# Kernel optimization log

Measured on AMD Instinct MI355X. Metric: run time of the kernel, lower is better.

The kernel has to match this reference:

```python
import jax, jax.numpy as jnp
import numpy as np

TOP_K = 2
TEMP = 0.9
EPS = 1e-5
B, S, D, F, E = 2, 2048, 1024, 4096, 8


def setup_inputs() -> dict:
    key = jax.random.key(0)
    ks = jax.random.split(key, 4)
    scale_in = 1.0 / np.sqrt(D)
    scale_ff = 1.0 / np.sqrt(F)
    return {
        "x": jax.random.normal(ks[0], (B, S, D), jnp.float32),
        "gate_w": jax.random.normal(ks[1], (D, E), jnp.float32) * scale_in,
        "gate_b": jnp.zeros((E,), jnp.float32),
        "w1": jax.random.normal(ks[2], (E, D, F), jnp.float32) * scale_in,
        "b1": jnp.zeros((E, F), jnp.float32),
        "w2": jax.random.normal(ks[3], (E, F, D), jnp.float32) * scale_ff,
        "b2": jnp.zeros((E, D), jnp.float32),
        "ln_g": jnp.ones((D,), jnp.float32),
        "ln_b": jnp.zeros((D,), jnp.float32),
    }


def _moe_forward(x, gate_w, gate_b, w1, b1, w2, b2, ln_g, ln_b):
    # Gating: top-k masked softmax over experts
    logits = (x @ gate_w + gate_b) / TEMP                       # [B,S,E]
    topk_vals, topk_idx = jax.lax.top_k(logits, TOP_K)          # [B,S,K]
    keep = jax.nn.one_hot(topk_idx, E, dtype=jnp.bool_).any(-2)  # [B,S,E]
    masked = jnp.where(keep, logits, -jnp.inf)
    gate_probs = jax.nn.softmax(masked, axis=-1)                # [B,S,E]

    # Dense all-expert FFN (faithful to the naive original)
    h = jnp.einsum('bsd,edf->bsef', x, w1) + b1                 # [B,S,E,F]
    h = jax.nn.gelu(h, approximate=False)
    expert_out = jnp.einsum('bsef,efd->bsed', h, w2) + b2       # [B,S,E,D]

    out = jnp.einsum('bse,bsed->bsd', gate_probs, expert_out)   # combine

    # Post LayerNorm (dropout is identity in eval)
    mu = out.mean(-1, keepdims=True)
    var = out.var(-1, keepdims=True)
    out = (out - mu) / jnp.sqrt(var + EPS) * ln_g + ln_b
    return out


def reference(x, gate_w, gate_b, w1, b1, w2, b2, ln_g, ln_b):
    return _moe_forward(x, gate_w, gate_b, w1, b1, w2, b2, ln_g, ln_b)
```

## Files before the change

kernel.cpp:

```cpp
#include <hip/hip_runtime.h>
#include <stdint.h>
#include <stddef.h>

#define T_TOK 4096
#define DD    1024
#define FF    4096
#define EE    8
#define MAXROWS 9216
#define MAXTILES 72

typedef unsigned short u16;
typedef unsigned int   u32;
typedef short  sh8 __attribute__((ext_vector_type(8)));
typedef __bf16 bf8 __attribute__((ext_vector_type(8)));
typedef float  fl4 __attribute__((ext_vector_type(4)));

__device__ __forceinline__ u32 f2b_u(float f){
  u32 u = __float_as_uint(f);
  return (u + 0x7FFFu + ((u >> 16) & 1u)) >> 16;
}
__device__ __forceinline__ u16 f2b(float f){ return (u16)f2b_u(f); }
__device__ __forceinline__ u32 pack2(float a, float b){ return f2b_u(a) | (f2b_u(b) << 16); }

__device__ __forceinline__ void gl_lds16(const u16* g, u16* l){
  __builtin_amdgcn_global_load_lds(
      (const __attribute__((address_space(1))) u32*)(g),
      (__attribute__((address_space(3))) u32*)(l), 16, 0, 0);
}

__device__ __forceinline__ fl4 mfma16(sh8 a, sh8 b, fl4 c){
  return __builtin_amdgcn_mfma_f32_16x16x32_bf16(
      __builtin_bit_cast(bf8, a), __builtin_bit_cast(bf8, b), c, 0, 0, 0);
}

__device__ __forceinline__ float gelu_f(float x){
  float x2 = x * x;
  float t  = fmaf(0.07135481283f, x2, 1.5957691216f);
  float u  = x * t;
  float e  = __expf(-u);
  return x * __frcp_rn(1.0f + e);
}

__global__ __launch_bounds__(256) void k_cvt_x(const float* __restrict__ x,
                                               u16* __restrict__ xb){
  size_t i = ((size_t)blockIdx.x * 256 + threadIdx.x) * 8;
  float4 a = *(const float4*)(x + i);
  float4 b = *(const float4*)(x + i + 4);
  uint4 v;
  v.x = pack2(a.x, a.y); v.y = pack2(a.z, a.w);
  v.z = pack2(b.x, b.y); v.w = pack2(b.z, b.w);
  *(uint4*)(xb + i) = v;
}

__global__ __launch_bounds__(256) void k_gate(const float* __restrict__ x,
    const float* __restrict__ gw, const float* __restrict__ gb,
    int* __restrict__ tidx, float* __restrict__ tp, int* __restrict__ meta){
  int lane = threadIdx.x & 63;
  int t = blockIdx.x * 4 + (threadIdx.x >> 6);
  const float* xr = x + (size_t)t * DD;
  float a0=0,a1=0,a2=0,a3=0,a4=0,a5=0,a6=0,a7=0;
  #pragma unroll
  for (int i = 0; i < 16; i++){
    int d = i * 64 + lane;
    float xv = xr[d];
    const float4* g4 = (const float4*)(gw + (size_t)d * EE);
    float4 p = g4[0], q = g4[1];
    a0 += xv*p.x; a1 += xv*p.y; a2 += xv*p.z; a3 += xv*p.w;
    a4 += xv*q.x; a5 += xv*q.y; a6 += xv*q.z; a7 += xv*q.w;
  }
  #pragma unroll
  for (int off = 32; off > 0; off >>= 1){
    a0 += __shfl_xor(a0, off, 64); a1 += __shfl_xor(a1, off, 64);
    a2 += __shfl_xor(a2, off, 64); a3 += __shfl_xor(a3, off, 64);
    a4 += __shfl_xor(a4, off, 64); a5 += __shfl_xor(a5, off, 64);
    a6 += __shfl_xor(a6, off, 64); a7 += __shfl_xor(a7, off, 64);
  }
  if (lane == 0){
    float l[8] = {a0,a1,a2,a3,a4,a5,a6,a7};
    #pragma unroll
    for (int e = 0; e < 8; e++) l[e] = (l[e] + gb[e]) * (1.0f / 0.9f);
    int i1 = 0;
    #pragma unroll
    for (int e = 1; e < 8; e++) if (l[e] > l[i1]) i1 = e;
    int i2 = (i1 == 0) ? 1 : 0;
    #pragma unroll
    for (int e = 0; e < 8; e++) if (e != i1 && l[e] > l[i2]) i2 = e;
    float ex = expf(l[i2] - l[i1]);
    float inv = 1.0f / (1.0f + ex);
    tidx[2*t] = i1; tidx[2*t+1] = i2;
    tp[2*t] = inv;  tp[2*t+1] = ex * inv;
    atomicAdd(&meta[i1], 1);
    atomicAdd(&meta[i2], 1);
  }
}

__global__ __launch_bounds__(256) void k_fillscan(const int* __restrict__ tidx,
    const float* __restrict__ tp, int* __restrict__ meta,
    int* __restrict__ rowmap, float* __restrict__ rowp){
  __shared__ int sbase[EE];
  __shared__ int scur[EE];
  int tid = threadIdx.x;
  if (tid < EE) scur[tid] = 0;
  if (tid == 0){
    int rowbase = 0, total = 0;
    for (int e = 0; e < EE; e++){
      int c = meta[e];
      sbase[e] = rowbase;
      int nt = (c + 127) >> 7;
      for (int i = 0; i < nt; i++){
        meta[32 + total]  = e;
        meta[104 + total] = rowbase + i * 128;
        total++;
      }
      rowbase += nt << 7;
    }
    meta[24] = total;
  }
  __syncthreads();
  for (int t = tid; t < T_TOK; t += 256){
    #pragma unroll
    for (int k = 0; k < 2; k++){
      int e = tidx[2*t + k];
      int pos = atomicAdd(&scur[e], 1);
      int row = sbase[e] + pos;
      rowmap[row] = (t << 1) | k;
      rowp[row] = tp[2*t + k];
    }
  }
}

__global__ __launch_bounds__(256) void k_cvtw(const float* __restrict__ src,
    u16* __restrict__ dst, int R, int C){
  __shared__ float tile[64][65];
  int e = blockIdx.z;
  const float* se = src + (size_t)e * R * C;
  u16* de = dst + (size_t)e * R * C;
  int rblk = blockIdx.y * 64, cblk = blockIdx.x * 64;
  int tid = threadIdx.x;
  int lr = tid >> 4, lc = tid & 15;
  #pragma unroll
  for (int i = 0; i < 4; i++){
    int row = lr + i * 16;
    float4 v = *(const float4*)(se + (size_t)(rblk + row) * C + cblk + lc * 4);
    tile[row][lc*4+0] = v.x; tile[row][lc*4+1] = v.y;
    tile[row][lc*4+2] = v.z; tile[row][lc*4+3] = v.w;
  }
  __syncthreads();
  int c = tid >> 2, seg = tid & 3;
  u32 o[8];
  #pragma unroll
  for (int j = 0; j < 8; j++){
    float f0 = tile[seg*16 + 2*j    ][c];
    float f1 = tile[seg*16 + 2*j + 1][c];
    o[j] = pack2(f0, f1);
  }
  u16* dp = de + (size_t)(cblk + c) * R + rblk + seg * 16;
  *(uint4*)(dp)     = make_uint4(o[0], o[1], o[2], o[3]);
  *(uint4*)(dp + 8) = make_uint4(o[4], o[5], o[6], o[7]);
}

__global__ __launch_bounds__(256) void k_gemm_h(
    const u16* __restrict__ Xb, const u16* __restrict__ Wt,
    const float* __restrict__ b1, const int* __restrict__ meta,
    const int* __restrict__ rowmap, u16* __restrict__ H){
  __shared__ u16 As[128 * 64];
  __shared__ u16 Bs[128 * 64];
  int tx = blockIdx.x;
  if (tx >= meta[24]) return;
  int e = meta[32 + tx], row0 = meta[104 + tx];
  int n0 = blockIdx.y * 128;
  int tid = threadIdx.x;
  int rsub = tid >> 3;
  int sw_st = ((tid & 7) ^ (rsub & 7)) * 8;
  const u16* Be = Wt + ((size_t)e * FF + n0) * DD;
  const u16* gA[4];
  const u16* gB[4];
  #pragma unroll
  for (int j = 0; j < 4; j++){
    int row = j * 32 + rsub;
    int rm = rowmap[row0 + row];
    int tok = (rm < 0) ? 0 : (rm >> 1);
    gA[j] = Xb + (size_t)tok * DD + sw_st;
    gB[j] = Be + (size_t)row * DD + sw_st;
  }
  u16* lA = As + tid * 8;
  u16* lB = Bs + tid * 8;

  int lane = tid & 63, wv = tid >> 6;
  int wm = wv & 1, wn = wv >> 1;
  int lr = lane & 15, lq = lane >> 4;
  int sw0 = ((lq    ) ^ (lr & 7)) * 8;
  int sw1 = ((lq + 4) ^ (lr & 7)) * 8;
  const u16* pA = As + (wm * 64 + lr) * 64;
  const u16* pB = Bs + (wn * 64 + lr) * 64;

  fl4 acc[4][4];
  #pragma unroll
  for (int mi = 0; mi < 4; mi++)
    #pragma unroll
    for (int ni = 0; ni < 4; ni++) acc[mi][ni] = (fl4){0.f,0.f,0.f,0.f};

  for (int k0 = 0; k0 < DD; k0 += 64){
    #pragma unroll
    for (int j = 0; j < 4; j++){
      gl_lds16(gA[j] + k0, lA + j * 2048);
      gl_lds16(gB[j] + k0, lB + j * 2048);
    }
    __syncthreads();
    #pragma unroll
    for (int kk = 0; kk < 2; kk++){
      int sw = kk ? sw1 : sw0;
      sh8 a[4], b[4];
      #pragma unroll
      for (int mi = 0; mi < 4; mi++) a[mi] = *(const sh8*)(pA + mi * 1024 + sw);
      #pragma unroll
      for (int ni = 0; ni < 4; ni++) b[ni] = *(const sh8*)(pB + ni * 1024 + sw);
      #pragma unroll
      for (int mi = 0; mi < 4; mi++)
        #pragma unroll
        for (int ni = 0; ni < 4; ni++)
          acc[mi][ni] = mfma16(a[mi], b[ni], acc[mi][ni]);
    }
    __syncthreads();
  }

  const float* b1e = b1 + (size_t)e * FF;
  float bias[4];
  #pragma unroll
  for (int ni = 0; ni < 4; ni++) bias[ni] = b1e[n0 + wn*64 + ni*16 + lr];
  #pragma unroll
  for (int mi = 0; mi < 4; mi++){
    int grb = row0 + wm * 64 + mi * 16 + lq * 4;
    #pragma unroll
    for (int ni = 0; ni < 4; ni++){
      int gc = n0 + wn * 64 + ni * 16 + lr;
      #pragma unroll
      for (int r = 0; r < 4; r++){
        float v = acc[mi][ni][r] + bias[ni];
        H[(size_t)(grb + r) * FF + gc] = f2b(gelu_f(v));
      }
    }
  }
}

__global__ __launch_bounds__(256) void k_gemm_y(
    const u16* __restrict__ H, const u16* __restrict__ Wt,
    const float* __restrict__ b2, const int* __restrict__ meta,
    const int* __restrict__ rowmap, const float* __restrict__ rowp,
    float* __restrict__ slots){
  __shared__ u16 As[128 * 64];
  __shared__ u16 Bs[128 * 64];
  int tx = blockIdx.x;
  if (tx >= meta[24]) return;
  int e = meta[32 + tx], row0 = meta[104 + tx];
  int n0 = blockIdx.y * 128;
  int tid = threadIdx.x;
  int rsub = tid >> 3;
  int sw_st = ((tid & 7) ^ (rsub & 7)) * 8;
  const u16* Be = Wt + ((size_t)e * DD + n0) * FF;
  const u16* gA[4];
  const u16* gB[4];
  #pragma unroll
  for (int j = 0; j < 4; j++){
    int row = j * 32 + rsub;
    gA[j] = H + (size_t)(row0 + row) * FF + sw_st;
    gB[j] = Be + (size_t)row * FF + sw_st;
  }
  u16* lA = As + tid * 8;
  u16* lB = Bs + tid * 8;

  int lane = tid & 63, wv = tid >> 6;
  int wm = wv & 1, wn = wv >> 1;
  int lr = lane & 15, lq = lane >> 4;
  int sw0 = ((lq    ) ^ (lr & 7)) * 8;
  int sw1 = ((lq + 4) ^ (lr & 7)) * 8;
  const u16* pA = As + (wm * 64 + lr) * 64;
  const u16* pB = Bs + (wn * 64 + lr) * 64;

  fl4 acc[4][4];
  #pragma unroll
  for (int mi = 0; mi < 4; mi++)
    #pragma unroll
    for (int ni = 0; ni < 4; ni++) acc[mi][ni] = (fl4){0.f,0.f,0.f,0.f};

  for (int k0 = 0; k0 < FF; k0 += 64){
    #pragma unroll
    for (int j = 0; j < 4; j++){
      gl_lds16(gA[j] + k0, lA + j * 2048);
      gl_lds16(gB[j] + k0, lB + j * 2048);
    }
    __syncthreads();
    #pragma unroll
    for (int kk = 0; kk < 2; kk++){
      int sw = kk ? sw1 : sw0;
      sh8 a[4], b[4];
      #pragma unroll
      for (int mi = 0; mi < 4; mi++) a[mi] = *(const sh8*)(pA + mi * 1024 + sw);
      #pragma unroll
      for (int ni = 0; ni < 4; ni++) b[ni] = *(const sh8*)(pB + ni * 1024 + sw);
      #pragma unroll
      for (int mi = 0; mi < 4; mi++)
        #pragma unroll
        for (int ni = 0; ni < 4; ni++)
          acc[mi][ni] = mfma16(a[mi], b[ni], acc[mi][ni]);
    }
    __syncthreads();
  }

  const float* b2e = b2 + (size_t)e * DD;
  float bias[4];
  #pragma unroll
  for (int ni = 0; ni < 4; ni++) bias[ni] = b2e[n0 + wn*64 + ni*16 + lr];
  #pragma unroll
  for (int mi = 0; mi < 4; mi++){
    int grb = row0 + wm * 64 + mi * 16 + lq * 4;
    #pragma unroll
    for (int r = 0; r < 4; r++){
      int gr = grb + r;
      int sl = rowmap[gr];
      if (sl < 0) continue;
      float p = rowp[gr];
      #pragma unroll
      for (int ni = 0; ni < 4; ni++){
        int gc = n0 + wn * 64 + ni * 16 + lr;
        slots[(size_t)sl * DD + gc] = (acc[mi][ni][r] + bias[ni]) * p;
      }
    }
  }
}

__global__ __launch_bounds__(256) void k_ln(const float* __restrict__ slots,
    const float* __restrict__ lng, const float* __restrict__ lnb,
    float* __restrict__ out){
  int lane = threadIdx.x & 63;
  int t = blockIdx.x * 4 + (threadIdx.x >> 6);
  const float* s0 = slots + (size_t)(2 * t) * DD;
  const float* s1 = s0 + DD;
  float y[16];
  float sum = 0.f, sq = 0.f;
  #pragma unroll
  for (int i = 0; i < 2; i++){
    int d = lane * 8 + i * 512;
    float4 p0 = *(const float4*)(s0 + d);
    float4 p1 = *(const float4*)(s0 + d + 4);
    float4 q0 = *(const float4*)(s1 + d);
    float4 q1 = *(const float4*)(s1 + d + 4);
    y[i*8+0]=p0.x+q0.x; y[i*8+1]=p0.y+q0.y; y[i*8+2]=p0.z+q0.z; y[i*8+3]=p0.w+q0.w;
    y[i*8+4]=p1.x+q1.x; y[i*8+5]=p1.y+q1.y; y[i*8+6]=p1.z+q1.z; y[i*8+7]=p1.w+q1.w;
  }
  #pragma unroll
  for (int j = 0; j < 16; j++){ sum += y[j]; sq += y[j]*y[j]; }
  #pragma unroll
  for (int off = 32; off > 0; off >>= 1){
    sum += __shfl_xor(sum, off, 64);
    sq  += __shfl_xor(sq,  off, 64);
  }
  float mu = sum * (1.0f / DD);
  float var = sq * (1.0f / DD) - mu * mu;
  float rs = 1.0f / sqrtf(var + 1e-5f);
  #pragma unroll
  for (int i = 0; i < 2; i++){
    int d = lane * 8 + i * 512;
    float4 g0 = *(const float4*)(lng + d), g1 = *(const float4*)(lng + d + 4);
    float4 c0 = *(const float4*)(lnb + d), c1 = *(const float4*)(lnb + d + 4);
    float4 o0, o1;
    o0.x=(y[i*8+0]-mu)*rs*g0.x+c0.x; o0.y=(y[i*8+1]-mu)*rs*g0.y+c0.y;
    o0.z=(y[i*8+2]-mu)*rs*g0.z+c0.z; o0.w=(y[i*8+3]-mu)*rs*g0.w+c0.w;
    o1.x=(y[i*8+4]-mu)*rs*g1.x+c1.x; o1.y=(y[i*8+5]-mu)*rs*g1.y+c1.y;
    o1.z=(y[i*8+6]-mu)*rs*g1.z+c1.z; o1.w=(y[i*8+7]-mu)*rs*g1.w+c1.w;
    *(float4*)(out + (size_t)t * DD + d)     = o0;
    *(float4*)(out + (size_t)t * DD + d + 4) = o1;
  }
}

extern "C" void kernel_launch(void* const* d_in, const int* in_sizes, int n_in,
                              void* d_out, int out_size, void* d_ws, size_t ws_size,
                              hipStream_t stream){
  const float* x   = (const float*)d_in[0];
  const float* gw  = (const float*)d_in[1];
  const float* gb  = (const float*)d_in[2];
  const float* w1  = (const float*)d_in[3];
  const float* b1  = (const float*)d_in[4];
  const float* w2  = (const float*)d_in[5];
  const float* b2  = (const float*)d_in[6];
  const float* lng = (const float*)d_in[7];
  const float* lnb = (const float*)d_in[8];
  float* out = (float*)d_out;

  char* ws = (char*)d_ws;
  size_t off = 0;
  auto alloc = [&](size_t bytes) -> void* {
    void* p = ws + off;
    off = (off + bytes + 255) & ~(size_t)255;
    return p;
  };
  int*   meta   = (int*)  alloc(256 * 4);
  int*   rowmap = (int*)  alloc(MAXROWS * 4);
  float* rowp   = (float*)alloc(MAXROWS * 4);
  int*   tidx   = (int*)  alloc(2 * T_TOK * 4);
  float* tp     = (float*)alloc(2 * T_TOK * 4);
  u16*   Xb     = (u16*)  alloc((size_t)T_TOK * DD * 2);
  float* slots  = (float*)alloc((size_t)T_TOK * 2 * DD * 4);
  u16*   H      = (u16*)  alloc((size_t)MAXROWS * FF * 2);
  u16*   Wt     = (u16*)  alloc((size_t)EE * DD * FF * 2);
  (void)ws_size; (void)in_sizes; (void)n_in; (void)out_size;

  hipMemsetAsync(meta, 0, 64, stream);
  hipMemsetAsync(rowmap, 0xFF, MAXROWS * 4, stream);

  k_cvt_x   <<<(T_TOK * DD) / (256 * 8), 256, 0, stream>>>(x, Xb);
  k_gate    <<<T_TOK / 4, 256, 0, stream>>>(x, gw, gb, tidx, tp, meta);
  k_fillscan<<<1, 256, 0, stream>>>(tidx, tp, meta, rowmap, rowp);

  k_cvtw  <<<dim3(FF / 64, DD / 64, EE), 256, 0, stream>>>(w1, Wt, DD, FF);
  k_gemm_h<<<dim3(MAXTILES, FF / 128), 256, 0, stream>>>(Xb, Wt, b1, meta, rowmap, H);
  k_cvtw  <<<dim3(DD / 64, FF / 64, EE), 256, 0, stream>>>(w2, Wt, FF, DD);
  k_gemm_y<<<dim3(MAXTILES, DD / 128), 256, 0, stream>>>(H, Wt, b2, meta, rowmap, rowp, slots);

  k_ln    <<<T_TOK / 4, 256, 0, stream>>>(slots, lng, lnb, out);
}
```

Measured before the change: 709.8 us.

## Fuse x conversion into gating, split-K second GEMM, reorder tile indexing

After: 633.1 us. -10.8%, faster.

```diff
diff --git a/kernel.cpp b/kernel.cpp
--- a/kernel.cpp
+++ b/kernel.cpp
@@ -41,20 +41,9 @@
   return x * __frcp_rn(1.0f + e);
 }
 
-__global__ __launch_bounds__(256) void k_cvt_x(const float* __restrict__ x,
-                                               u16* __restrict__ xb){
-  size_t i = ((size_t)blockIdx.x * 256 + threadIdx.x) * 8;
-  float4 a = *(const float4*)(x + i);
-  float4 b = *(const float4*)(x + i + 4);
-  uint4 v;
-  v.x = pack2(a.x, a.y); v.y = pack2(a.z, a.w);
-  v.z = pack2(b.x, b.y); v.w = pack2(b.z, b.w);
-  *(uint4*)(xb + i) = v;
-}
-
-__global__ __launch_bounds__(256) void k_gate(const float* __restrict__ x,
+__global__ __launch_bounds__(256) void k_gate_cvt(const float* __restrict__ x,
     const float* __restrict__ gw, const float* __restrict__ gb,
-    int* __restrict__ tidx, float* __restrict__ tp, int* __restrict__ meta){
+    int* __restrict__ tidx, float* __restrict__ tp, u16* __restrict__ xb){
   int lane = threadIdx.x & 63;
   int t = blockIdx.x * 4 + (threadIdx.x >> 6);
   const float* xr = x + (size_t)t * DD;
@@ -68,6 +57,20 @@
     a0 += xv*p.x; a1 += xv*p.y; a2 += xv*p.z; a3 += xv*p.w;
     a4 += xv*q.x; a5 += xv*q.y; a6 += xv*q.z; a7 += xv*q.w;
   }
+  {
+    int db = lane * 16;
+    float4 va = *(const float4*)(xr + db);
+    float4 vb = *(const float4*)(xr + db + 4);
+    float4 vc = *(const float4*)(xr + db + 8);
+    float4 vd = *(const float4*)(xr + db + 12);
+    uint4 o0, o1;
+    o0.x = pack2(va.x, va.y); o0.y = pack2(va.z, va.w);
+    o0.z = pack2(vb.x, vb.y); o0.w = pack2(vb.z, vb.w);
+    o1.x = pack2(vc.x, vc.y); o1.y = pack2(vc.z, vc.w);
+    o1.z = pack2(vd.x, vd.y); o1.w = pack2(vd.z, vd.w);
+    *(uint4*)(xb + (size_t)t * DD + db)     = o0;
+    *(uint4*)(xb + (size_t)t * DD + db + 8) = o1;
+  }
   #pragma unroll
   for (int off = 32; off > 0; off >>= 1){
     a0 += __shfl_xor(a0, off, 64); a1 += __shfl_xor(a1, off, 64);
@@ -89,24 +92,25 @@
     float inv = 1.0f / (1.0f + ex);
     tidx[2*t] = i1; tidx[2*t+1] = i2;
     tp[2*t] = inv;  tp[2*t+1] = ex * inv;
-    atomicAdd(&meta[i1], 1);
-    atomicAdd(&meta[i2], 1);
   }
 }
 
 __global__ __launch_bounds__(256) void k_fillscan(const int* __restrict__ tidx,
     const float* __restrict__ tp, int* __restrict__ meta,
     int* __restrict__ rowmap, float* __restrict__ rowp){
+  __shared__ int hist[EE];
   __shared__ int sbase[EE];
   __shared__ int scur[EE];
   int tid = threadIdx.x;
-  if (tid < EE) scur[tid] = 0;
+  if (tid < EE){ hist[tid] = 0; scur[tid] = 0; }
+  __syncthreads();
+  for (int i = tid; i < 2 * T_TOK; i += 256) atomicAdd(&hist[tidx[i]], 1);
+  __syncthreads();
   if (tid == 0){
     int rowbase = 0, total = 0;
     for (int e = 0; e < EE; e++){
-      int c = meta[e];
       sbase[e] = rowbase;
-      int nt = (c + 127) >> 7;
+      int nt = (hist[e] + 127) >> 7;
       for (int i = 0; i < nt; i++){
         meta[32 + total]  = e;
         meta[104 + total] = rowbase + i * 128;
@@ -116,6 +120,7 @@
     }
     meta[24] = total;
   }
+  for (int r = tid; r < MAXROWS; r += 256) rowmap[r] = -1;
   __syncthreads();
   for (int t = tid; t < T_TOK; t += 256){
     #pragma unroll
@@ -165,10 +170,12 @@
     const int* __restrict__ rowmap, u16* __restrict__ H){
   __shared__ u16 As[128 * 64];
   __shared__ u16 Bs[128 * 64];
-  int tx = blockIdx.x;
+  int id = blockIdx.y * MAXTILES + blockIdx.x;
+  int tx  = id >> 5;
+  int nty = id & 31;
   if (tx >= meta[24]) return;
   int e = meta[32 + tx], row0 = meta[104 + tx];
-  int n0 = blockIdx.y * 128;
+  int n0 = nty * 128;
   int tid = threadIdx.x;
   int rsub = tid >> 3;
   int sw_st = ((tid & 7) ^ (rsub & 7)) * 8;
@@ -250,20 +257,24 @@
     float* __restrict__ slots){
   __shared__ u16 As[128 * 64];
   __shared__ u16 Bs[128 * 64];
-  int tx = blockIdx.x;
+  int id = blockIdx.y * MAXTILES + blockIdx.x;
+  int tx  = id >> 3;
+  int nty = id & 7;
   if (tx >= meta[24]) return;
   int e = meta[32 + tx], row0 = meta[104 + tx];
-  int n0 = blockIdx.y * 128;
+  int n0 = nty * 128;
+  int kz = blockIdx.z;
+  int kbase = kz * (FF / 2);
   int tid = threadIdx.x;
   int rsub = tid >> 3;
   int sw_st = ((tid & 7) ^ (rsub & 7)) * 8;
-  const u16* Be = Wt + ((size_t)e * DD + n0) * FF;
+  const u16* Be = Wt + ((size_t)e * DD + n0) * FF + kbase;
   const u16* gA[4];
   const u16* gB[4];
   #pragma unroll
   for (int j = 0; j < 4; j++){
     int row = j * 32 + rsub;
-    gA[j] = H + (size_t)(row0 + row) * FF + sw_st;
+    gA[j] = H + (size_t)(row0 + row) * FF + kbase + sw_st;
     gB[j] = Be + (size_t)row * FF + sw_st;
   }
   u16* lA = As + tid * 8;
@@ -283,7 +294,8 @@
     #pragma unroll
     for (int ni = 0; ni < 4; ni++) acc[mi][ni] = (fl4){0.f,0.f,0.f,0.f};
 
-  for (int k0 = 0; k0 < FF; k0 += 64){
+  const int KC = FF / 2;
+  for (int k0 = 0; k0 < KC; k0 += 64){
     #pragma unroll
     for (int j = 0; j < 4; j++){
       gl_lds16(gA[j] + k0, lA + j * 2048);
@@ -310,7 +322,8 @@
   const float* b2e = b2 + (size_t)e * DD;
   float bias[4];
   #pragma unroll
-  for (int ni = 0; ni < 4; ni++) bias[ni] = b2e[n0 + wn*64 + ni*16 + lr];
+  for (int ni = 0; ni < 4; ni++)
+    bias[ni] = (kz == 0) ? b2e[n0 + wn*64 + ni*16 + lr] : 0.0f;
   #pragma unroll
   for (int mi = 0; mi < 4; mi++){
     int grb = row0 + wm * 64 + mi * 16 + lq * 4;
@@ -323,7 +336,7 @@
       #pragma unroll
       for (int ni = 0; ni < 4; ni++){
         int gc = n0 + wn * 64 + ni * 16 + lr;
-        slots[(size_t)sl * DD + gc] = (acc[mi][ni][r] + bias[ni]) * p;
+        atomicAdd(&slots[(size_t)sl * DD + gc], (acc[mi][ni][r] + bias[ni]) * p);
       }
     }
   }
@@ -405,17 +418,15 @@
   u16*   Wt     = (u16*)  alloc((size_t)EE * DD * FF * 2);
   (void)ws_size; (void)in_sizes; (void)n_in; (void)out_size;
 
-  hipMemsetAsync(meta, 0, 64, stream);
-  hipMemsetAsync(rowmap, 0xFF, MAXROWS * 4, stream);
-
-  k_cvt_x   <<<(T_TOK * DD) / (256 * 8), 256, 0, stream>>>(x, Xb);
-  k_gate    <<<T_TOK / 4, 256, 0, stream>>>(x, gw, gb, tidx, tp, meta);
+  hipMemsetAsync(slots, 0, (size_t)T_TOK * 2 * DD * 4, stream);
+
+  k_gate_cvt<<<T_TOK / 4, 256, 0, stream>>>(x, gw, gb, tidx, tp, Xb);
   k_fillscan<<<1, 256, 0, stream>>>(tidx, tp, meta, rowmap, rowp);
 
   k_cvtw  <<<dim3(FF / 64, DD / 64, EE), 256, 0, stream>>>(w1, Wt, DD, FF);
   k_gemm_h<<<dim3(MAXTILES, FF / 128), 256, 0, stream>>>(Xb, Wt, b1, meta, rowmap, H);
   k_cvtw  <<<dim3(DD / 64, FF / 64, EE), 256, 0, stream>>>(w2, Wt, FF, DD);
-  k_gemm_y<<<dim3(MAXTILES, DD / 128), 256, 0, stream>>>(H, Wt, b2, meta, rowmap, rowp, slots);
+  k_gemm_y<<<dim3(MAXTILES, DD / 128, 2), 256, 0, stream>>>(H, Wt, b2, meta, rowmap, rowp, slots);
 
   k_ln    <<<T_TOK / 4, 256, 0, stream>>>(slots, lng, lnb, out);
 }
```
